# Performance work log

Measured on AMD Instinct MI355X. Metric: run time of the kernel, lower is better.

The kernel has to match this reference:

```python
import jax, jax.numpy as jnp
import numpy as np

GLYPH_DIM = 4096
PADDING_IDX = GLYPH_DIM  # 4096
GLYPH_EMB = 20           # CHAR_EMB 16 + COLOR_EMB 4
HIDDEN = 32
MAX_LEN = 64


def setup_inputs() -> dict:
    key = jax.random.key(0)
    k1, k2, k3, k4, k5, k6, k7 = jax.random.split(key, 7)
    B, H, W = 8192, 21, 79
    glyph_chars = jax.random.randint(k1, (B, H, W), 0, 256, dtype=jnp.int32)
    glyph_colors = jax.random.randint(k2, (B, H, W), 0, 16, dtype=jnp.int32)
    # Embedding table with zero padding row (torch padding_idx semantics)
    emb_table = jax.random.normal(k3, (GLYPH_DIM + 1, GLYPH_EMB), dtype=jnp.float32) * 0.02
    emb_table = emb_table.at[PADDING_IDX].set(0.0)
    s = 1.0 / np.sqrt(HIDDEN)
    W_ih = jax.random.uniform(k4, (HIDDEN, GLYPH_EMB), minval=-s, maxval=s, dtype=jnp.float32)
    W_hh = jax.random.uniform(k5, (HIDDEN, HIDDEN), minval=-s, maxval=s, dtype=jnp.float32)
    b_ih = jax.random.uniform(k6, (HIDDEN,), minval=-s, maxval=s, dtype=jnp.float32)
    b_hh = jax.random.uniform(k7, (HIDDEN,), minval=-s, maxval=s, dtype=jnp.float32)
    return {"glyph_chars": glyph_chars, "glyph_colors": glyph_colors,
            "emb_table": emb_table, "W_ih": W_ih, "W_hh": W_hh,
            "b_ih": b_ih, "b_hh": b_hh}


def _encode_bag(glyph_chars, glyph_colors):
    """Batched sorted-unique compaction over the bounded glyph id range."""
    B = glyph_chars.shape[0]
    g_ids = ((glyph_chars << 4) + glyph_colors).reshape(B, -1)  # [B, H*W]
    # presence[b, g] = glyph g appears in sample b (batched histogram)
    bidx = jnp.broadcast_to(jnp.arange(B, dtype=g_ids.dtype)[:, None], g_ids.shape)
    presence = jnp.zeros((B, GLYPH_DIM), dtype=bool).at[bidx, g_ids].set(True)
    # compact: present ids keep their value, absent become PADDING_IDX (=4096),
    # so sorting yields ascending unique ids followed by padding.
    ids = jnp.arange(GLYPH_DIM, dtype=jnp.int32)
    keys = jnp.where(presence, ids, jnp.int32(PADDING_IDX))
    bag = jnp.sort(keys, axis=1)[:, :MAX_LEN]  # [B, MAX_LEN]
    lengths = jnp.minimum(presence.sum(axis=1), MAX_LEN)  # [B]
    return bag, lengths


def reference(glyph_chars, glyph_colors, emb_table, W_ih, W_hh, b_ih, b_hh):
    bag, lengths = _encode_bag(glyph_chars, glyph_colors)
    emb = emb_table[bag]  # [B, MAX_LEN, GLYPH_EMB]
    B = emb.shape[0]

    # packed RNN == plain RNN where hidden state freezes past each sequence length
    xs = jnp.swapaxes(emb, 0, 1)  # [T, B, E]

    def step(h, inp):
        xt, t = inp
        h_new = jnp.tanh(xt @ W_ih.T + b_ih + h @ W_hh.T + b_hh)
        h = jnp.where((t < lengths)[:, None], h_new, h)
        return h, None

    h0 = jnp.zeros((B, HIDDEN), dtype=emb.dtype)
    h, _ = jax.lax.scan(step, h0, (xs, jnp.arange(MAX_LEN)))
    return (h, emb, bag)
```

## Files before the change

### kernel.cpp

```cpp
#include <hip/hip_runtime.h>

#define HW 1659
#define PADID 4096
#define EMB 20
#define HID 32
#define MAXLEN 64

__global__ __launch_bounds__(128) void proj_kernel(
    const float* __restrict__ emb_table, const float* __restrict__ W_ih,
    float* __restrict__ proj)
{
    const int tid = threadIdx.x;
    const int g = blockIdx.x * 4 + (tid >> 5);
    const int j = tid & 31;
    if (g > PADID) return;
    const float* er = emb_table + (size_t)g * EMB;
    const float* wr = W_ih + j * EMB;
    float s = 0.f;
#pragma unroll
    for (int k = 0; k < EMB; k++) s += wr[k] * er[k];
    proj[(size_t)g * HID + j] = s;
}

__global__ __launch_bounds__(256) void bag_emb_kernel(
    const int* __restrict__ chars, const int* __restrict__ colors,
    const float* __restrict__ emb_table,
    float* __restrict__ out_emb, float* __restrict__ out_bag)
{
    __shared__ unsigned char pres[4096];
    __shared__ int bagl[64];
    __shared__ int wsum[4];

    const int b   = blockIdx.x;
    const int tid = threadIdx.x;
    const int lane = tid & 63;
    const int wv   = tid >> 6;

    ((uint4*)pres)[tid] = make_uint4(0u, 0u, 0u, 0u);
    if (tid < 64) bagl[tid] = PADID;
    __syncthreads();

    const int base = b * HW;
    const int pe = (4 - (base & 3)) & 3;
    if (tid < pe) {
        int g = (chars[base + tid] << 4) + colors[base + tid];
        pres[g] = 1;
    }
    const int nv = (HW - pe) >> 2;
    const int nt = HW - pe - (nv << 2);
    const int4* c4 = (const int4*)(chars + base + pe);
    const int4* k4 = (const int4*)(colors + base + pe);
    for (int v = tid; v < nv; v += 256) {
        int4 c = c4[v], k = k4[v];
        pres[(c.x << 4) + k.x] = 1;
        pres[(c.y << 4) + k.y] = 1;
        pres[(c.z << 4) + k.z] = 1;
        pres[(c.w << 4) + k.w] = 1;
    }
    if (tid < nt) {
        int i = base + pe + (nv << 2) + tid;
        pres[(chars[i] << 4) + colors[i]] = 1;
    }
    __syncthreads();

    uint4 w4 = ((const uint4*)pres)[tid];
    const unsigned M = 0x01010101u;
    int cnt = __popc(w4.x & M) + __popc(w4.y & M)
            + __popc(w4.z & M) + __popc(w4.w & M);

    int pre = cnt;
#pragma unroll
    for (int d = 1; d < 64; d <<= 1) {
        int v = __shfl_up(pre, d, 64);
        if (lane >= d) pre += v;
    }
    if (lane == 63) wsum[wv] = pre;
    __syncthreads();
    int wbase = 0;
#pragma unroll
    for (int w2 = 0; w2 < 4; w2++) wbase += (w2 < wv) ? wsum[w2] : 0;
    int p = wbase + pre - cnt;

    unsigned wrd[4] = {w4.x, w4.y, w4.z, w4.w};
#pragma unroll
    for (int c = 0; c < 4; c++) {
#pragma unroll
        for (int k = 0; k < 4; k++) {
            if ((wrd[c] >> (8 * k)) & 1) {
                if (p < 64) bagl[p] = 16 * tid + 4 * c + k;
                p++;
            }
        }
    }
    __syncthreads();

    if (tid < 64) out_bag[(size_t)b * 64 + tid] = (float)bagl[tid];

    const float4* tab4 = (const float4*)emb_table;
    float4* dst4 = (float4*)(out_emb + (size_t)b * (MAXLEN * EMB));
    for (int q = tid; q < MAXLEN * 5; q += 256) {
        int t = q / 5;
        int m = q - t * 5;
        int row = bagl[t];
        dst4[q] = tab4[row * 5 + m];
    }
}

__global__ __launch_bounds__(128, 4) void rnn_kernel(
    const float* __restrict__ proj, const float* __restrict__ bagf,
    const float* __restrict__ W_hh,
    const float* __restrict__ b_ih, const float* __restrict__ b_hh,
    float* __restrict__ out_h)
{
    __shared__ float hbuf[4][32];

    const int tid = threadIdx.x;
    const int ib  = tid >> 5;
    const int j   = tid & 31;
    const int b   = blockIdx.x * 4 + ib;

    float whh[HID];
#pragma unroll
    for (int k = 0; k < HID; k++) whh[k] = W_hh[j * HID + k];
    const float sbias = b_ih[j] + b_hh[j];

    const float* bp = bagf + (size_t)b * 64;
    unsigned long long m0 = __ballot(bp[j]      < 4095.5f);
    unsigned long long m1 = __ballot(bp[32 + j] < 4095.5f);
    const int half = ib & 1;
    const int len = __popc((unsigned)(m0 >> (half * 32)))
                  + __popc((unsigned)(m1 >> (half * 32)));

    hbuf[ib][j] = 0.f;
    asm volatile("s_waitcnt lgkmcnt(0)" ::: "memory");

    float h = 0.f;
    for (int t = 0; t < MAXLEN; t++) {
        const int idx = (int)bp[t];
        const float pv = proj[(size_t)idx * HID + j];

        float s = sbias + pv;
        const float4* hb4 = (const float4*)hbuf[ib];
#pragma unroll
        for (int m = 0; m < 8; m++) {
            float4 hv = hb4[m];
            s += whh[4*m+0]*hv.x + whh[4*m+1]*hv.y
               + whh[4*m+2]*hv.z + whh[4*m+3]*hv.w;
        }

        s = fminf(fmaxf(s, -9.f), 9.f);
        float e = __expf(2.f * s);
        float th = (e - 1.f) * __builtin_amdgcn_rcpf(e + 1.f);

        h = (t < len) ? th : h;

        hbuf[ib][j] = h;
        asm volatile("s_waitcnt lgkmcnt(0)" ::: "memory");
    }

    out_h[(size_t)b * HID + j] = h;
}

__global__ __launch_bounds__(128, 4) void rnn_kernel_noproj(
    const float* __restrict__ emb, const float* __restrict__ bagf,
    const float* __restrict__ W_ih, const float* __restrict__ W_hh,
    const float* __restrict__ b_ih, const float* __restrict__ b_hh,
    float* __restrict__ out_h)
{
    __shared__ float hbuf[4][32];
    const int tid = threadIdx.x;
    const int ib  = tid >> 5;
    const int j   = tid & 31;
    const int b   = blockIdx.x * 4 + ib;

    float wih[EMB];
#pragma unroll
    for (int k = 0; k < EMB; k++) wih[k] = W_ih[j * EMB + k];
    float whh[HID];
#pragma unroll
    for (int k = 0; k < HID; k++) whh[k] = W_hh[j * HID + k];
    const float sbias = b_ih[j] + b_hh[j];

    const float* bp = bagf + (size_t)b * 64;
    unsigned long long m0 = __ballot(bp[j]      < 4095.5f);
    unsigned long long m1 = __ballot(bp[32 + j] < 4095.5f);
    const int half = ib & 1;
    const int len = __popc((unsigned)(m0 >> (half * 32)))
                  + __popc((unsigned)(m1 >> (half * 32)));

    hbuf[ib][j] = 0.f;
    asm volatile("s_waitcnt lgkmcnt(0)" ::: "memory");

    float h = 0.f;
    const float* xb = emb + (size_t)b * (MAXLEN * EMB);
    for (int t = 0; t < MAXLEN; t++) {
        const float4* xp = (const float4*)(xb + t * EMB);
        float4 x0 = xp[0], x1 = xp[1], x2 = xp[2], x3 = xp[3], x4 = xp[4];
        float s = sbias;
        const float4* hb4 = (const float4*)hbuf[ib];
#pragma unroll
        for (int m = 0; m < 8; m++) {
            float4 hv = hb4[m];
            s += whh[4*m+0]*hv.x + whh[4*m+1]*hv.y
               + whh[4*m+2]*hv.z + whh[4*m+3]*hv.w;
        }
        s += wih[0]*x0.x + wih[1]*x0.y + wih[2]*x0.z + wih[3]*x0.w;
        s += wih[4]*x1.x + wih[5]*x1.y + wih[6]*x1.z + wih[7]*x1.w;
        s += wih[8]*x2.x + wih[9]*x2.y + wih[10]*x2.z + wih[11]*x2.w;
        s += wih[12]*x3.x + wih[13]*x3.y + wih[14]*x3.z + wih[15]*x3.w;
        s += wih[16]*x4.x + wih[17]*x4.y + wih[18]*x4.z + wih[19]*x4.w;
        s = fminf(fmaxf(s, -9.f), 9.f);
        float e = __expf(2.f * s);
        float th = (e - 1.f) * __builtin_amdgcn_rcpf(e + 1.f);
        h = (t < len) ? th : h;
        hbuf[ib][j] = h;
        asm volatile("s_waitcnt lgkmcnt(0)" ::: "memory");
    }
    out_h[(size_t)b * HID + j] = h;
}

extern "C" void kernel_launch(void* const* d_in, const int* in_sizes, int n_in,
                              void* d_out, int out_size, void* d_ws, size_t ws_size,
                              hipStream_t stream) {
    const int*   chars     = (const int*)d_in[0];
    const int*   colors    = (const int*)d_in[1];
    const float* emb_table = (const float*)d_in[2];
    const float* W_ih      = (const float*)d_in[3];
    const float* W_hh      = (const float*)d_in[4];
    const float* b_ih      = (const float*)d_in[5];
    const float* b_hh      = (const float*)d_in[6];

    const int B = in_sizes[0] / HW;

    float* out     = (float*)d_out;
    float* out_h   = out;
    float* out_emb = out + (size_t)B * HID;
    float* out_bag = out_emb + (size_t)B * MAXLEN * EMB;

    const size_t proj_bytes = (size_t)(PADID + 1) * HID * sizeof(float);

    bag_emb_kernel<<<B, 256, 0, stream>>>(chars, colors, emb_table, out_emb, out_bag);

    if (ws_size >= proj_bytes) {
        float* proj = (float*)d_ws;
        proj_kernel<<<(PADID + 1 + 3) / 4, 128, 0, stream>>>(emb_table, W_ih, proj);
        rnn_kernel<<<B / 4, 128, 0, stream>>>(proj, out_bag, W_hh, b_ih, b_hh, out_h);
    } else {
        rnn_kernel_noproj<<<B / 4, 128, 0, stream>>>(out_emb, out_bag, W_ih, W_hh,
                                                     b_ih, b_hh, out_h);
    }
}
```

Baseline: 196.1 us.

## Compute two hidden units per thread in RNN kernel, eight samples per block

Each thread of the recurrent kernel now computes two hidden units (j and j+16) instead of one, so a 128-thread block processes eight samples instead of four and the grid is halved. The hidden state is stored in shared memory in an interleaved float2 layout, and W_hh rows are loaded with a permuted column order to match it. Each shared-memory float4 read of h now feeds two dot products, and the accumulation is split into two partial sums to shorten dependency chains. The cost is twice the weight registers per thread (64 floats) and fewer threads overall, which may reduce latency hiding on the serial 64-step loop.

```diff
diff --git a/kernel.cpp b/kernel.cpp
--- a/kernel.cpp
+++ b/kernel.cpp
@@ -112,53 +112,75 @@
     const float* __restrict__ b_ih, const float* __restrict__ b_hh,
     float* __restrict__ out_h)
 {
-    __shared__ float hbuf[4][32];
-
-    const int tid = threadIdx.x;
-    const int ib  = tid >> 5;
-    const int j   = tid & 31;
-    const int b   = blockIdx.x * 4 + ib;
-
-    float whh[HID];
-#pragma unroll
-    for (int k = 0; k < HID; k++) whh[k] = W_hh[j * HID + k];
-    const float sbias = b_ih[j] + b_hh[j];
-
-    const float* bp = bagf + (size_t)b * 64;
-    unsigned long long m0 = __ballot(bp[j]      < 4095.5f);
-    unsigned long long m1 = __ballot(bp[32 + j] < 4095.5f);
-    const int half = ib & 1;
-    const int len = __popc((unsigned)(m0 >> (half * 32)))
-                  + __popc((unsigned)(m1 >> (half * 32)));
-
-    hbuf[ib][j] = 0.f;
+    __shared__ float hbuf[8][32];
+
+    const int tid  = threadIdx.x;
+    const int wv   = tid >> 6;
+    const int lane = tid & 63;
+    const int sl   = lane >> 4;
+    const int ib   = wv * 4 + sl;
+    const int jj   = lane & 15;
+    const int b    = blockIdx.x * 8 + ib;
+
+    float w0[HID], w1[HID];
+#pragma unroll
+    for (int k = 0; k < HID; k++) {
+        const int src = ((k & 1) << 4) + (k >> 1);
+        w0[k] = W_hh[jj * HID + src];
+        w1[k] = W_hh[(jj + 16) * HID + src];
+    }
+    const float sb0 = b_ih[jj] + b_hh[jj];
+    const float sb1 = b_ih[jj + 16] + b_hh[jj + 16];
+
+    const float* bps = bagf + (size_t)b * 64;
+
+    unsigned long long mm0 = __ballot(bps[jj]      < 4095.5f);
+    unsigned long long mm1 = __ballot(bps[jj + 16] < 4095.5f);
+    unsigned long long mm2 = __ballot(bps[jj + 32] < 4095.5f);
+    unsigned long long mm3 = __ballot(bps[jj + 48] < 4095.5f);
+    const int sh = sl * 16;
+    const int len = __popc((unsigned)((mm0 >> sh) & 0xFFFFu))
+                  + __popc((unsigned)((mm1 >> sh) & 0xFFFFu))
+                  + __popc((unsigned)((mm2 >> sh) & 0xFFFFu))
+                  + __popc((unsigned)((mm3 >> sh) & 0xFFFFu));
+
+    ((float2*)hbuf[ib])[jj] = make_float2(0.f, 0.f);
     asm volatile("s_waitcnt lgkmcnt(0)" ::: "memory");
 
-    float h = 0.f;
+    float h0 = 0.f, h1 = 0.f;
     for (int t = 0; t < MAXLEN; t++) {
-        const int idx = (int)bp[t];
-        const float pv = proj[(size_t)idx * HID + j];
-
-        float s = sbias + pv;
+        const int idx = (int)bps[t];
+        const float pv0 = proj[idx * HID + jj];
+        const float pv1 = proj[idx * HID + jj + 16];
+
         const float4* hb4 = (const float4*)hbuf[ib];
-#pragma unroll
-        for (int m = 0; m < 8; m++) {
-            float4 hv = hb4[m];
-            s += whh[4*m+0]*hv.x + whh[4*m+1]*hv.y
-               + whh[4*m+2]*hv.z + whh[4*m+3]*hv.w;
+        float a0 = sb0 + pv0, a1 = sb1 + pv1, c0 = 0.f, c1 = 0.f;
+#pragma unroll
+        for (int m = 0; m < 8; m += 2) {
+            float4 u = hb4[m], v = hb4[m + 1];
+            a0 += w0[4*m+0]*u.x + w0[4*m+1]*u.y + w0[4*m+2]*u.z + w0[4*m+3]*u.w;
+            a1 += w1[4*m+0]*u.x + w1[4*m+1]*u.y + w1[4*m+2]*u.z + w1[4*m+3]*u.w;
+            c0 += w0[4*m+4]*v.x + w0[4*m+5]*v.y + w0[4*m+6]*v.z + w0[4*m+7]*v.w;
+            c1 += w1[4*m+4]*v.x + w1[4*m+5]*v.y + w1[4*m+6]*v.z + w1[4*m+7]*v.w;
         }
-
-        s = fminf(fmaxf(s, -9.f), 9.f);
-        float e = __expf(2.f * s);
-        float th = (e - 1.f) * __builtin_amdgcn_rcpf(e + 1.f);
-
-        h = (t < len) ? th : h;
-
-        hbuf[ib][j] = h;
+        float s0 = a0 + c0, s1 = a1 + c1;
+
+        s0 = fminf(fmaxf(s0, -9.f), 9.f);
+        s1 = fminf(fmaxf(s1, -9.f), 9.f);
+        float e0 = __expf(2.f * s0);
+        float e1 = __expf(2.f * s1);
+        float th0 = (e0 - 1.f) * __builtin_amdgcn_rcpf(e0 + 1.f);
+        float th1 = (e1 - 1.f) * __builtin_amdgcn_rcpf(e1 + 1.f);
+
+        h0 = (t < len) ? th0 : h0;
+        h1 = (t < len) ? th1 : h1;
+
+        ((float2*)hbuf[ib])[jj] = make_float2(h0, h1);
         asm volatile("s_waitcnt lgkmcnt(0)" ::: "memory");
     }
 
-    out_h[(size_t)b * HID + j] = h;
+    out_h[(size_t)b * HID + jj]      = h0;
+    out_h[(size_t)b * HID + jj + 16] = h1;
 }
 
 __global__ __launch_bounds__(128, 4) void rnn_kernel_noproj(
@@ -244,7 +266,7 @@
     if (ws_size >= proj_bytes) {
         float* proj = (float*)d_ws;
         proj_kernel<<<(PADID + 1 + 3) / 4, 128, 0, stream>>>(emb_table, W_ih, proj);
-        rnn_kernel<<<B / 4, 128, 0, stream>>>(proj, out_bag, W_hh, b_ih, b_hh, out_h);
+        rnn_kernel<<<B / 8, 128, 0, stream>>>(proj, out_bag, W_hh, b_ih, b_hh, out_h);
     } else {
         rnn_kernel_noproj<<<B / 4, 128, 0, stream>>>(out_emb, out_bag, W_ih, W_hh,
                                                      b_ih, b_hh, out_h);
```

Result: no change. 194.5 us (-0.8%).
